# Kernel optimization log

Measured on AMD Instinct MI355X. Metric: run time of the kernel, lower is better.

## Reference

```python
import jax, jax.numpy as jnp
import numpy as np
from jax import lax

EPS = 1e-5


def _st_gcn_layer(x, w, b, A):
    # x: (N, C, T, V); w: (K*Co, C, 9, 1); A: (K, V, V) (already scaled by edge importance)
    y = lax.conv_general_dilated(x, w, window_strides=(1, 1),
                                 padding=[(4, 4), (0, 0)],
                                 dimension_numbers=('NCHW', 'OIHW', 'NCHW'))
    y = y + b[None, :, None, None]
    N, KC, T, V = y.shape
    K = A.shape[0]
    y = y.reshape(N, K, KC // K, T, V)
    y = jnp.einsum('nkctv,kvw->nctw', y, A)  # graph convolution
    return jax.nn.relu(y)


def setup_inputs() -> dict:
    key = jax.random.key(0)
    ks = jax.random.split(key, 8)
    N, T, V, C, Co, K, KT = 16, 512, 25, 256, 256, 3, 9
    x = jax.random.normal(ks[0], (N, T, V, C), dtype=jnp.float32)
    bn_gamma = jax.random.uniform(ks[1], (V * C,), dtype=jnp.float32)
    bn_beta = jax.random.normal(ks[2], (V * C,), dtype=jnp.float32)
    bn_mean = jnp.zeros((V * C,), dtype=jnp.float32)
    bn_var = jnp.ones((V * C,), dtype=jnp.float32)
    w_scale = 1.0 / np.sqrt(C * KT)
    w1 = jax.random.normal(ks[3], (K * Co, C, KT, 1), dtype=jnp.float32) * w_scale
    b1 = jax.random.normal(ks[4], (K * Co,), dtype=jnp.float32) * 0.01
    w2 = jax.random.normal(ks[5], (K * Co, Co, KT, 1), dtype=jnp.float32) * w_scale
    b2 = jax.random.normal(ks[6], (K * Co,), dtype=jnp.float32) * 0.01
    ei1 = jnp.ones((K, V, V), dtype=jnp.float32)
    ei2 = jnp.ones((K, V, V), dtype=jnp.float32)
    A = jax.random.uniform(ks[7], (K, V, V), dtype=jnp.float32)
    return {"x": x, "bn_gamma": bn_gamma, "bn_beta": bn_beta, "bn_mean": bn_mean,
            "bn_var": bn_var, "w1": w1, "b1": b1, "ei1": ei1, "w2": w2, "b2": b2,
            "ei2": ei2, "A": A}


def reference(x, bn_gamma, bn_beta, bn_mean, bn_var, w1, b1, ei1, w2, b2, ei2, A):
    N, T, V, C = x.shape
    # data_bn over V*C channels (V-major, C-minor per the torch permutes), eval mode
    xb = jnp.transpose(x, (0, 2, 3, 1)).reshape(N, V * C, T)  # (N, V*C, T)
    inv = bn_gamma / jnp.sqrt(bn_var + EPS)
    xb = (xb - bn_mean[None, :, None]) * inv[None, :, None] + bn_beta[None, :, None]
    xb = jnp.transpose(xb.reshape(N, V, C, T), (0, 2, 3, 1))  # (N, C, T, V)
    h = _st_gcn_layer(xb, w1, b1, A * ei1)
    h = _st_gcn_layer(h, w2, b2, A * ei2)
    return jnp.transpose(h, (0, 2, 3, 1))  # (N, T, V, Cout)
```

## Files before the change

kernel.cpp:

```cpp
#include <hip/hip_runtime.h>
#include <stdint.h>

typedef unsigned short ushortT;
typedef short short8 __attribute__((ext_vector_type(8)));
typedef float f32x4 __attribute__((ext_vector_type(4)));
typedef float f32x2 __attribute__((ext_vector_type(2)));
typedef unsigned short us4 __attribute__((ext_vector_type(4)));

#define TP 520
#define PAD 4
#define XPAD_B 20480
#define ATILE_B 8192

__device__ __forceinline__ unsigned short f2bf(float f) {
  union { float f; unsigned int u; } v; v.f = f;
  unsigned int r = (v.u + 0x7fffu + ((v.u >> 16) & 1u)) >> 16;
  return (unsigned short)r;
}
__device__ __forceinline__ float bf2f(unsigned short b) {
  union { unsigned int u; float f; } v; v.u = ((unsigned int)b) << 16;
  return v.f;
}
__device__ __forceinline__ float ldadp(const void* p, long i, int bf) {
  return bf ? bf2f(((const unsigned short*)p)[i]) : ((const float*)p)[i];
}
__device__ __forceinline__ f32x2 ldadp2(const void* p, long i, int bf) {
  f32x2 r;
  if (bf) {
    unsigned int u = *(const unsigned int*)((const unsigned short*)p + i);
    r[0] = bf2f((unsigned short)(u & 0xffffu));
    r[1] = bf2f((unsigned short)(u >> 16));
  } else {
    r = *(const f32x2*)((const float*)p + i);
  }
  return r;
}

__device__ __forceinline__ void gload16(const void* g, void* l) {
  __builtin_amdgcn_global_load_lds(
      (const __attribute__((address_space(1))) void*)g,
      (__attribute__((address_space(3))) void*)l, 16, 0, 0);
}

__global__ void detect_kernel(const void* var, int* flags) {
  flags[0] = (((const unsigned int*)var)[0] == 0x3F803F80u) ? 1 : 0;
}

__global__ void prep_w_kernel(const void* w, ushortT* __restrict__ Wt, const int* flags) {
  int bf = flags[0];
  long i = (long)blockIdx.x * 256 + threadIdx.x;
  int c = (int)(i & 255);
  long mc = i >> 8;
  int m = (int)(mc % 768);
  int dt = (int)(mc / 768);
  long dst = (((long)(dt * 8 + (c >> 5)) * 768 + m) << 5) + (c & 31);
  Wt[dst] = f2bf(ldadp(w, ((long)m * 256 + c) * 9 + dt, bf));
}

__global__ void prep_ae_kernel(const void* A, const void* ei, const void* b,
                               float* __restrict__ Ae, float* __restrict__ Bsum,
                               const int* flags) {
  __shared__ float ash[1875];
  int bf = flags[0];
  int tid = threadIdx.x;
  for (int i = tid; i < 1875; i += 1024) {
    float ae = ldadp(A, i, bf) * ldadp(ei, i, bf);
    ash[i] = ae; Ae[i] = ae;
  }
  __syncthreads();
  for (int i = tid; i < 6400; i += 1024) {
    int c = i / 25, w = i % 25;
    float s = 0.f;
    for (int k = 0; k < 3; k++) {
      float cs = 0.f;
      for (int v = 0; v < 25; v++) cs += ash[(k * 25 + v) * 25 + w];
      s += ldadp(b, k * 256 + c, bf) * cs;
    }
    Bsum[i] = s;
  }
}

__global__ void pad_kernel(ushortT* __restrict__ Xb) {
  long nv = (long)blockIdx.y * 25 + blockIdx.x;
  int tid = threadIdx.x;
  #pragma unroll
  for (int r = 0; r < 4; r++) {
    Xb[(nv * TP + r) * 256 + tid] = 0;
    Xb[(nv * TP + 516 + r) * 256 + tid] = 0;
  }
}

__global__ void bn_kernel(const void* x, long xoff, const void* gamma, const void* beta,
                          const void* mean, const void* var, const int* flags,
                          ushortT* __restrict__ Xb, long total) {
  long i2 = ((long)blockIdx.x * 256 + threadIdx.x) * 2;
  if (i2 >= total) return;
  int bf = flags[0];
  int c = (int)(i2 & 255);
  long j = i2 >> 8;
  int v = (int)(j % 25); j /= 25;
  int t = (int)(j % 512); j /= 512;
  int nl = (int)j;
  int pc = v * 256 + c;
  f32x2 xv = ldadp2(x, xoff + i2, bf);
  unsigned int outw = 0;
  #pragma unroll
  for (int e = 0; e < 2; e++) {
    float inv = ldadp(gamma, pc + e, bf) * rsqrtf(ldadp(var, pc + e, bf) + 1e-5f);
    float val = (xv[e] - ldadp(mean, pc + e, bf)) * inv + ldadp(beta, pc + e, bf);
    outw |= ((unsigned int)f2bf(val)) << (16 * e);
  }
  *(unsigned int*)(Xb + (((long)(nl * 25 + v)) * TP + t + PAD) * 256 + c) = outw;
}

__global__ __launch_bounds__(256, 2) void conv_kernel(
    const ushortT* __restrict__ Xb, const ushortT* __restrict__ Wt,
    ushortT* __restrict__ Y) {
  __shared__ short8 smem[(2 * XPAD_B + 3 * ATILE_B) / 16];
  char* lds = (char*)smem;
  char* Xl0 = lds;
  char* Xl1 = lds + XPAD_B;
  char* Ap0 = lds + 2 * XPAD_B;
  char* Ap1 = Ap0 + ATILE_B;
  char* Ap2 = Ap0 + 2 * ATILE_B;

  const int tid = threadIdx.x;
  const int lane = tid & 63;
  const int wave = tid >> 6;
  const int wm = wave >> 1, wn = wave & 1;
  const int kb = lane >> 4;
  const int l15 = lane & 15;
  const int wubase = (tid & ~63);

  int bid = blockIdx.x;
  const int v = bid % 25;
  const int rtile = bid / 25;
  const int tt = rtile & 1;
  const int mt = rtile >> 1;
  const int nl = blockIdx.y;
  const int m0 = mt * 128;
  const int t0 = tt * 256;

  const long xrowbase = ((long)(nl * 25 + v)) * TP + t0;

  auto stageX = [&](int cc, char* xb) {
    #pragma unroll
    for (int k = 0; k < 5; k++) {
      int s = k * 256 + tid;
      int r = s >> 2, q = s & 3;
      if (k == 4) r = (r < 264) ? r : 263;
      int ql = q ^ ((r >> 1) & 3);
      gload16(Xb + (xrowbase + r) * 256 + cc * 32 + ql * 8,
              xb + (long)(k * 256 + wubase) * 16);
    }
  };
  auto stageA = [&](int g, char* ab) {
    const ushortT* wb = Wt + (((long)g * 768 + m0) << 5);
    #pragma unroll
    for (int k = 0; k < 2; k++) {
      int s = k * 256 + tid;
      int r = s >> 2, q = s & 3;
      int ql = q ^ ((r >> 1) & 3);
      gload16(wb + (long)(r * 4 + ql) * 8, ab + (long)(k * 256 + wubase) * 16);
    }
  };

  f32x4 acc[4][8];
  #pragma unroll
  for (int i = 0; i < 4; i++)
    #pragma unroll
    for (int j = 0; j < 8; j++) { acc[i][j][0]=0.f; acc[i][j][1]=0.f; acc[i][j][2]=0.f; acc[i][j][3]=0.f; }

  stageX(0, Xl0);
  stageA(0, Ap0);
  stageA(8, Ap1);

  for (int cc = 0; cc < 8; cc++) {
    char* Xcur = (cc & 1) ? Xl1 : Xl0;
    char* Xnext = (cc & 1) ? Xl0 : Xl1;
    #pragma unroll
    for (int dt = 0; dt < 9; dt++) {
      if (dt == 8) { asm volatile("s_waitcnt vmcnt(7)" ::: "memory"); }
      else         { asm volatile("s_waitcnt vmcnt(2)" ::: "memory"); }
      __builtin_amdgcn_s_barrier();

      if (dt <= 6) {
        stageA((dt + 2) * 8 + cc, (dt + 2) % 3 == 0 ? Ap0 : ((dt + 2) % 3 == 1 ? Ap1 : Ap2));
      } else if (dt == 7) {
        stageA(cc + 1, Ap0);
        stageX(cc + 1, Xnext);
      } else {
        stageA(8 + cc + 1, Ap1);
      }

      const char* Acur = (dt % 3 == 0) ? Ap0 : ((dt % 3 == 1) ? Ap1 : Ap2);
      short8 a[4], b[8];
      #pragma unroll
      for (int i = 0; i < 4; i++) {
        int r = wm * 64 + i * 16 + l15;
        int sl = kb ^ ((r >> 1) & 3);
        a[i] = *(const short8*)(Acur + r * 64 + sl * 16);
      }
      #pragma unroll
      for (int j = 0; j < 8; j++) {
        int r = wn * 128 + j * 16 + l15 + dt;
        int sl = kb ^ ((r >> 1) & 3);
        b[j] = *(const short8*)(Xcur + r * 64 + sl * 16);
      }
      #pragma unroll
      for (int i = 0; i < 4; i++)
        #pragma unroll
        for (int j = 0; j < 8; j++)
          acc[i][j] = __builtin_amdgcn_mfma_f32_16x16x32_bf16(a[i], b[j], acc[i][j], 0, 0, 0);
    }
  }

  #pragma unroll
  for (int i = 0; i < 4; i++) {
    #pragma unroll
    for (int j = 0; j < 8; j++) {
      int tg = t0 + wn * 128 + j * 16 + l15;
      int kc = m0 + wm * 64 + i * 16 + (kb << 2);
      long off = (((long)(nl * 512 + tg)) * 25 + v) * 768 + kc;
      us4 u;
      u[0] = f2bf(acc[i][j][0]);
      u[1] = f2bf(acc[i][j][1]);
      u[2] = f2bf(acc[i][j][2]);
      u[3] = f2bf(acc[i][j][3]);
      *(us4*)(Y + off) = u;
    }
  }
}

__global__ __launch_bounds__(256) void gconv_kernel(
    const ushortT* __restrict__ Y, const float* __restrict__ Ae,
    const float* __restrict__ Bsum, ushortT* __restrict__ dstb,
    float* __restrict__ dstf, int mode) {
  __shared__ float aesh[1875];
  const int tid = threadIdx.x;
  const int cp = tid & 127;
  const int c  = cp * 2;
  const int th = tid >> 7;
  const int nl = blockIdx.y;
  const int t0 = blockIdx.x << 2;
  const int tA = t0 + 2 * th;
  for (int i = tid; i < 1875; i += 256) aesh[i] = Ae[i];
  __syncthreads();

  float acc[2][2][25];
  #pragma unroll
  for (int w = 0; w < 25; w++) {
    float b0 = Bsum[c * 25 + w], b1 = Bsum[(c + 1) * 25 + w];
    acc[0][0][w] = b0; acc[0][1][w] = b0;
    acc[1][0][w] = b1; acc[1][1][w] = b1;
  }
  for (int k = 0; k < 3; k++) {
    for (int v = 0; v < 25; v++) {
      long ybase = (((long)(nl * 512 + tA)) * 25 + v) * 768 + k * 256 + c;
      unsigned int ua = *(const unsigned int*)(Y + ybase);
      unsigned int ub = *(const unsigned int*)(Y + ybase + 25L * 768);
      float ya0 = bf2f((unsigned short)(ua & 0xffffu));
      float ya1 = bf2f((unsigned short)(ua >> 16));
      float yb0 = bf2f((unsigned short)(ub & 0xffffu));
      float yb1 = bf2f((unsigned short)(ub >> 16));
      const float* ap = &aesh[(k * 25 + v) * 25];
      #pragma unroll
      for (int w = 0; w < 25; w++) {
        float a = ap[w];
        acc[0][0][w] = fmaf(ya0, a, acc[0][0][w]);
        acc[1][0][w] = fmaf(ya1, a, acc[1][0][w]);
        acc[0][1][w] = fmaf(yb0, a, acc[0][1][w]);
        acc[1][1][w] = fmaf(yb1, a, acc[1][1][w]);
      }
    }
  }
  #pragma unroll
  for (int tt = 0; tt < 2; tt++) {
    int t = tA + tt;
    #pragma unroll
    for (int w = 0; w < 25; w++) {
      float v0 = acc[0][tt][w]; v0 = v0 > 0.f ? v0 : 0.f;
      float v1 = acc[1][tt][w]; v1 = v1 > 0.f ? v1 : 0.f;
      if (mode == 0) {
        unsigned int pk = (unsigned int)f2bf(v0) | ((unsigned int)f2bf(v1) << 16);
        *(unsigned int*)(dstb + (((long)(nl * 25 + w)) * TP + t + PAD) * 256 + c) = pk;
      } else {
        f32x2 pk; pk[0] = v0; pk[1] = v1;
        *(f32x2*)(dstf + (((long)(nl * 512 + t)) * 25 + w) * 256 + c) = pk;
      }
    }
  }
}

extern "C" void kernel_launch(void* const* d_in, const int* in_sizes, int n_in,
                              void* d_out, int out_size, void* d_ws, size_t ws_size,
                              hipStream_t stream) {
  const void* x     = d_in[0];
  const void* gamma = d_in[1];
  const void* beta  = d_in[2];
  const void* mean  = d_in[3];
  const void* var   = d_in[4];
  const void* w1    = d_in[5];
  const void* b1    = d_in[6];
  const void* ei1   = d_in[7];
  const void* w2    = d_in[8];
  const void* b2    = d_in[9];
  const void* ei2   = d_in[10];
  const void* A     = d_in[11];
  float* out = (float*)d_out;

  const size_t WtB  = 9L * 768 * 256 * 2;
  const size_t XbB1 = 25L * TP * 256 * 2;
  const size_t YB1  = 512L * 25 * 768 * 2;
  const size_t fixed = 256 + 2 * WtB + 2 * (1875 * 4) + 2 * (6400 * 4) + 8 * 256;

  int G = 16;
  while (G > 1 && fixed + (size_t)G * (XbB1 + YB1) > ws_size) G >>= 1;

  char* ws = (char*)d_ws;
  size_t off = 0;
  auto alloc = [&](size_t bytes) { char* p = ws + off; off = (off + bytes + 255) & ~(size_t)255; return p; };
  int* flags   = (int*)alloc(256);
  ushortT* Wt1 = (ushortT*)alloc(WtB);
  ushortT* Wt2 = (ushortT*)alloc(WtB);
  float* Ae1   = (float*)alloc(1875 * 4);
  float* Ae2   = (float*)alloc(1875 * 4);
  float* Bs1   = (float*)alloc(6400 * 4);
  float* Bs2   = (float*)alloc(6400 * 4);
  ushortT* Xb  = (ushortT*)alloc((size_t)G * XbB1);
  ushortT* Y   = (ushortT*)alloc((size_t)G * YB1);

  detect_kernel<<<1, 1, 0, stream>>>(var, flags);
  prep_w_kernel<<<6912, 256, 0, stream>>>(w1, Wt1, flags);
  prep_w_kernel<<<6912, 256, 0, stream>>>(w2, Wt2, flags);
  prep_ae_kernel<<<1, 1024, 0, stream>>>(A, ei1, b1, Ae1, Bs1, flags);
  prep_ae_kernel<<<1, 1024, 0, stream>>>(A, ei2, b2, Ae2, Bs2, flags);

  for (int n0 = 0; n0 < 16; n0 += G) {
    long xoff = (long)n0 * 512 * 25 * 256;
    float* out_c = out + (size_t)n0 * 512 * 25 * 256;
    long total = (long)G * 512 * 25 * 256;

    pad_kernel<<<dim3(25, G), 256, 0, stream>>>(Xb);
    bn_kernel<<<(int)((total / 2 + 255) / 256), 256, 0, stream>>>(x, xoff, gamma, beta, mean, var, flags, Xb, total);

    conv_kernel<<<dim3(300, G), 256, 0, stream>>>(Xb, Wt1, Y);
    gconv_kernel<<<dim3(128, G), 256, 0, stream>>>(Y, Ae1, Bs1, Xb, (float*)nullptr, 0);
    conv_kernel<<<dim3(300, G), 256, 0, stream>>>(Xb, Wt2, Y);
    gconv_kernel<<<dim3(128, G), 256, 0, stream>>>(Y, Ae2, Bs2, (ushortT*)nullptr, out_c, 1);
  }
}
```

Before: 1.694 ms.

## Widen BN and graph-conv memory accesses to 4 elements and raise MFMA priority

The batch-norm kernel now handles four channels per thread, using 64-bit bf16 or 128-bit fp32 loads and a 64-bit store. The graph-conv kernel is remapped so each thread owns four channels at one time step, which gives wider Y loads and output stores. The conv kernel raises wave priority around the MFMA block with s_setprio. The wider accesses cut instruction count, but the gconv remap changes how reuse and coalescing fall across the wave.

```diff
diff --git a/kernel.cpp b/kernel.cpp
--- a/kernel.cpp
+++ b/kernel.cpp
@@ -23,17 +23,6 @@
 }
 __device__ __forceinline__ float ldadp(const void* p, long i, int bf) {
   return bf ? bf2f(((const unsigned short*)p)[i]) : ((const float*)p)[i];
-}
-__device__ __forceinline__ f32x2 ldadp2(const void* p, long i, int bf) {
-  f32x2 r;
-  if (bf) {
-    unsigned int u = *(const unsigned int*)((const unsigned short*)p + i);
-    r[0] = bf2f((unsigned short)(u & 0xffffu));
-    r[1] = bf2f((unsigned short)(u >> 16));
-  } else {
-    r = *(const f32x2*)((const float*)p + i);
-  }
-  return r;
 }
 
 __device__ __forceinline__ void gload16(const void* g, void* l) {
@@ -93,24 +82,33 @@
 __global__ void bn_kernel(const void* x, long xoff, const void* gamma, const void* beta,
                           const void* mean, const void* var, const int* flags,
                           ushortT* __restrict__ Xb, long total) {
-  long i2 = ((long)blockIdx.x * 256 + threadIdx.x) * 2;
-  if (i2 >= total) return;
+  long i4 = ((long)blockIdx.x * 256 + threadIdx.x) * 4;
+  if (i4 >= total) return;
   int bf = flags[0];
-  int c = (int)(i2 & 255);
-  long j = i2 >> 8;
+  int c = (int)(i4 & 255);
+  long j = i4 >> 8;
   int v = (int)(j % 25); j /= 25;
   int t = (int)(j % 512); j /= 512;
   int nl = (int)j;
   int pc = v * 256 + c;
-  f32x2 xv = ldadp2(x, xoff + i2, bf);
-  unsigned int outw = 0;
-  #pragma unroll
-  for (int e = 0; e < 2; e++) {
+  float xv[4];
+  if (bf) {
+    us4 u = *(const us4*)((const ushortT*)x + xoff + i4);
+    #pragma unroll
+    for (int e = 0; e < 4; e++) xv[e] = bf2f(u[e]);
+  } else {
+    f32x4 u = *(const f32x4*)((const float*)x + xoff + i4);
+    #pragma unroll
+    for (int e = 0; e < 4; e++) xv[e] = u[e];
+  }
+  us4 outw;
+  #pragma unroll
+  for (int e = 0; e < 4; e++) {
     float inv = ldadp(gamma, pc + e, bf) * rsqrtf(ldadp(var, pc + e, bf) + 1e-5f);
     float val = (xv[e] - ldadp(mean, pc + e, bf)) * inv + ldadp(beta, pc + e, bf);
-    outw |= ((unsigned int)f2bf(val)) << (16 * e);
-  }
-  *(unsigned int*)(Xb + (((long)(nl * 25 + v)) * TP + t + PAD) * 256 + c) = outw;
+    outw[e] = f2bf(val);
+  }
+  *(us4*)(Xb + (((long)(nl * 25 + v)) * TP + t + PAD) * 256 + c) = outw;
 }
 
 __global__ __launch_bounds__(256, 2) void conv_kernel(
@@ -207,11 +205,13 @@
         int sl = kb ^ ((r >> 1) & 3);
         b[j] = *(const short8*)(Xcur + r * 64 + sl * 16);
       }
+      __builtin_amdgcn_s_setprio(1);
       #pragma unroll
       for (int i = 0; i < 4; i++)
         #pragma unroll
         for (int j = 0; j < 8; j++)
           acc[i][j] = __builtin_amdgcn_mfma_f32_16x16x32_bf16(a[i], b[j], acc[i][j], 0, 0, 0);
+      __builtin_amdgcn_s_setprio(0);
     }
   }
 
@@ -238,56 +238,45 @@
     float* __restrict__ dstf, int mode) {
   __shared__ float aesh[1875];
   const int tid = threadIdx.x;
-  const int cp = tid & 127;
-  const int c  = cp * 2;
-  const int th = tid >> 7;
+  const int c  = (tid & 63) * 4;
+  const int t  = (blockIdx.x << 2) + (tid >> 6);
   const int nl = blockIdx.y;
-  const int t0 = blockIdx.x << 2;
-  const int tA = t0 + 2 * th;
   for (int i = tid; i < 1875; i += 256) aesh[i] = Ae[i];
   __syncthreads();
 
-  float acc[2][2][25];
-  #pragma unroll
-  for (int w = 0; w < 25; w++) {
-    float b0 = Bsum[c * 25 + w], b1 = Bsum[(c + 1) * 25 + w];
-    acc[0][0][w] = b0; acc[0][1][w] = b0;
-    acc[1][0][w] = b1; acc[1][1][w] = b1;
-  }
+  float acc[4][25];
+  #pragma unroll
+  for (int e = 0; e < 4; e++)
+    #pragma unroll
+    for (int w = 0; w < 25; w++) acc[e][w] = Bsum[(c + e) * 25 + w];
+
   for (int k = 0; k < 3; k++) {
     for (int v = 0; v < 25; v++) {
-      long ybase = (((long)(nl * 512 + tA)) * 25 + v) * 768 + k * 256 + c;
-      unsigned int ua = *(const unsigned int*)(Y + ybase);
-      unsigned int ub = *(const unsigned int*)(Y + ybase + 25L * 768);
-      float ya0 = bf2f((unsigned short)(ua & 0xffffu));
-      float ya1 = bf2f((unsigned short)(ua >> 16));
-      float yb0 = bf2f((unsigned short)(ub & 0xffffu));
-      float yb1 = bf2f((unsigned short)(ub >> 16));
+      us4 u = *(const us4*)(Y + (((long)(nl * 512 + t)) * 25 + v) * 768 + k * 256 + c);
+      float y0 = bf2f(u[0]), y1 = bf2f(u[1]), y2 = bf2f(u[2]), y3 = bf2f(u[3]);
       const float* ap = &aesh[(k * 25 + v) * 25];
       #pragma unroll
       for (int w = 0; w < 25; w++) {
         float a = ap[w];
-        acc[0][0][w] = fmaf(ya0, a, acc[0][0][w]);
-        acc[1][0][w] = fmaf(ya1, a, acc[1][0][w]);
-        acc[0][1][w] = fmaf(yb0, a, acc[0][1][w]);
-        acc[1][1][w] = fmaf(yb1, a, acc[1][1][w]);
+        acc[0][w] = fmaf(y0, a, acc[0][w]);
+        acc[1][w] = fmaf(y1, a, acc[1][w]);
+        acc[2][w] = fmaf(y2, a, acc[2][w]);
+        acc[3][w] = fmaf(y3, a, acc[3][w]);
       }
     }
   }
   #pragma unroll
-  for (int tt = 0; tt < 2; tt++) {
-    int t = tA + tt;
-    #pragma unroll
-    for (int w = 0; w < 25; w++) {
-      float v0 = acc[0][tt][w]; v0 = v0 > 0.f ? v0 : 0.f;
-      float v1 = acc[1][tt][w]; v1 = v1 > 0.f ? v1 : 0.f;
-      if (mode == 0) {
-        unsigned int pk = (unsigned int)f2bf(v0) | ((unsigned int)f2bf(v1) << 16);
-        *(unsigned int*)(dstb + (((long)(nl * 25 + w)) * TP + t + PAD) * 256 + c) = pk;
-      } else {
-        f32x2 pk; pk[0] = v0; pk[1] = v1;
-        *(f32x2*)(dstf + (((long)(nl * 512 + t)) * 25 + w) * 256 + c) = pk;
-      }
+  for (int w = 0; w < 25; w++) {
+    float v0 = acc[0][w]; v0 = v0 > 0.f ? v0 : 0.f;
+    float v1 = acc[1][w]; v1 = v1 > 0.f ? v1 : 0.f;
+    float v2 = acc[2][w]; v2 = v2 > 0.f ? v2 : 0.f;
+    float v3 = acc[3][w]; v3 = v3 > 0.f ? v3 : 0.f;
+    if (mode == 0) {
+      us4 pk; pk[0] = f2bf(v0); pk[1] = f2bf(v1); pk[2] = f2bf(v2); pk[3] = f2bf(v3);
+      *(us4*)(dstb + (((long)(nl * 25 + w)) * TP + t + PAD) * 256 + c) = pk;
+    } else {
+      f32x4 pk; pk[0] = v0; pk[1] = v1; pk[2] = v2; pk[3] = v3;
+      *(f32x4*)(dstf + (((long)(nl * 512 + t)) * 25 + w) * 256 + c) = pk;
     }
   }
 }
@@ -342,7 +331,7 @@
     long total = (long)G * 512 * 25 * 256;
 
     pad_kernel<<<dim3(25, G), 256, 0, stream>>>(Xb);
-    bn_kernel<<<(int)((total / 2 + 255) / 256), 256, 0, stream>>>(x, xoff, gamma, beta, mean, var, flags, Xb, total);
+    bn_kernel<<<(int)((total / 4 + 255) / 256), 256, 0, stream>>>(x, xoff, gamma, beta, mean, var, flags, Xb, total);
 
     conv_kernel<<<dim3(300, G), 256, 0, stream>>>(Xb, Wt1, Y);
     gconv_kernel<<<dim3(128, G), 256, 0, stream>>>(Y, Ae1, Bs1, Xb, (float*)nullptr, 0);
```

New measurement: 1.749 ms. +3.2%, slower.
